# Performance work log

Measured on AMD Instinct MI355X. Metric: run time of the kernel, lower is better.

## Reference

```python
import jax, jax.numpy as jnp
import numpy as np

B, N, IN_DIM, OUT_DIM, H = 4, 2048, 1024, 1024, 16
HEAD_DIM = OUT_DIM // H  # 64


def setup_inputs() -> dict:
    key = jax.random.key(0)
    k_x, k_q, k_k, k_v, k_o = jax.random.split(key, 5)
    s = 1.0 / np.sqrt(IN_DIM)
    return {
        "x": jax.random.normal(k_x, (B, N, IN_DIM), dtype=jnp.float32),
        "w_q": jax.random.normal(k_q, (IN_DIM, OUT_DIM), dtype=jnp.float32) * s,
        "w_k": jax.random.normal(k_k, (IN_DIM, OUT_DIM), dtype=jnp.float32) * s,
        "w_v": jax.random.normal(k_v, (IN_DIM, OUT_DIM), dtype=jnp.float32) * s,
        "w_out": jax.random.normal(k_o, (OUT_DIM, OUT_DIM), dtype=jnp.float32) * s,
    }


def reference(x, w_q, w_k, w_v, w_out):
    b, n, _ = x.shape
    scale = 1.0 / jnp.sqrt(jnp.float32(HEAD_DIM))
    # QKV projections, split into heads: [b, h, n, d]
    q = (x @ w_q).reshape(b, n, H, HEAD_DIM).transpose(0, 2, 1, 3)
    k = (x @ w_k).reshape(b, n, H, HEAD_DIM).transpose(0, 2, 1, 3)
    v = (x @ w_v).reshape(b, n, H, HEAD_DIM).transpose(0, 2, 1, 3)
    # full score matrix [b, h, q, k]
    scores = jnp.einsum("bhqd,bhkd->bhqk", q, k) * scale
    # NOTE: source applies softmax over dim=1 (the HEAD axis) — reproduce exactly
    attn = jax.nn.softmax(scores, axis=1)
    # dropout p=0.0 -> identity
    ctx = jnp.einsum("bhqk,bhkd->bqhd", attn, v).reshape(b, n, OUT_DIM)
    return ctx @ w_out
```

## Files before the change

kernel.cpp:

```cpp
#include <hip/hip_runtime.h>
#include <hip/hip_bf16.h>

typedef unsigned short u16;
typedef unsigned int u32;
typedef __attribute__((ext_vector_type(8))) short short8;
typedef __attribute__((ext_vector_type(4))) float float4v;
typedef __attribute__((ext_vector_type(4))) unsigned int uint4v;

__device__ __forceinline__ u16 f2bf(float f) {
    union { float f; unsigned int u; } v; v.f = f;
    unsigned int r = v.u + 0x7fffu + ((v.u >> 16) & 1u);
    return (u16)(r >> 16);
}
__device__ __forceinline__ float bf2f(u16 h) {
    union { unsigned int u; float f; } v; v.u = ((unsigned int)h) << 16;
    return v.f;
}

__device__ __forceinline__ void gld_lds16(const u16* g, u16* l) {
    __builtin_amdgcn_global_load_lds(
        (const __attribute__((address_space(1))) u32*)g,
        (__attribute__((address_space(3))) u32*)l, 16, 0, 0);
}

__global__ __launch_bounds__(256) void convert_x(
    const float* __restrict__ x, u16* __restrict__ xb) {
    int i = (blockIdx.x * 256 + threadIdx.x) * 8;
    float4v a = *(const float4v*)&x[i];
    float4v b = *(const float4v*)&x[i + 4];
    u16 tmp[8] __attribute__((aligned(16)));
#pragma unroll
    for (int j = 0; j < 4; ++j) { tmp[j] = f2bf(a[j]); tmp[4 + j] = f2bf(b[j]); }
    *(uint4v*)&xb[i] = *(uint4v*)tmp;
}

__global__ __launch_bounds__(256) void transpose_w(
    const float* __restrict__ w0, const float* __restrict__ w1,
    const float* __restrict__ w2, const float* __restrict__ w3,
    u16* __restrict__ o0, u16* __restrict__ o1,
    u16* __restrict__ o2, u16* __restrict__ o3) {
    __shared__ u16 t[32][33];
    int z = blockIdx.z;
    const float* w = (z == 0) ? w0 : (z == 1) ? w1 : (z == 2) ? w2 : w3;
    u16* o         = (z == 0) ? o0 : (z == 1) ? o1 : (z == 2) ? o2 : o3;
    int bx = blockIdx.x * 32;
    int by = blockIdx.y * 32;
    int x = threadIdx.x, y = threadIdx.y;
#pragma unroll
    for (int i = 0; i < 4; ++i)
        t[y + i * 8][x] = f2bf(w[(size_t)(by + y + i * 8) * 1024 + bx + x]);
    __syncthreads();
#pragma unroll
    for (int i = 0; i < 4; ++i)
        o[(size_t)(bx + y + i * 8) * 1024 + by + x] = t[x][y + i * 8];
}

__global__ __launch_bounds__(256) void gemm_bt(
    const u16* __restrict__ A, const u16* __restrict__ Bt,
    void* __restrict__ Cout, int M, int N, int K, int mode) {
    __shared__ __attribute__((aligned(16))) u16 As[128 * 32];
    __shared__ __attribute__((aligned(16))) u16 Bs[128 * 32];
    const int tid = threadIdx.x;
    const int m0 = blockIdx.y * 128;
    const int n0 = blockIdx.x * 128;
    const int wid = tid >> 6;
    const int lane = tid & 63;
    const int ln = lane & 15, kq = lane >> 4;
    const int wm = (wid >> 1) * 64, wn = (wid & 1) * 64;

    float4v acc[4][4] = {};
    for (int k0 = 0; k0 < K; k0 += 32) {
#pragma unroll
        for (int i = 0; i < 2; ++i) {
            int chunk = tid + i * 256;
            int row = chunk >> 2, cg = chunk & 3;
            u16* lA = &As[(size_t)(i * 256 + wid * 64) * 8];
            u16* lB = &Bs[(size_t)(i * 256 + wid * 64) * 8];
            gld_lds16(&A[(size_t)(m0 + row) * K + k0 + cg * 8], lA);
            gld_lds16(&Bt[(size_t)(n0 + row) * K + k0 + cg * 8], lB);
        }
        __syncthreads();
        short8 af[4], bfr[4];
#pragma unroll
        for (int mt = 0; mt < 4; ++mt)
            af[mt] = *(const short8*)&As[(wm + mt * 16 + ln) * 32 + kq * 8];
#pragma unroll
        for (int nt = 0; nt < 4; ++nt)
            bfr[nt] = *(const short8*)&Bs[(wn + nt * 16 + ln) * 32 + kq * 8];
#pragma unroll
        for (int mt = 0; mt < 4; ++mt)
#pragma unroll
            for (int nt = 0; nt < 4; ++nt)
                acc[mt][nt] = __builtin_amdgcn_mfma_f32_16x16x32_bf16(
                    af[mt], bfr[nt], acc[mt][nt], 0, 0, 0);
        __syncthreads();
    }
    if (mode == 0) {
        u16* C = (u16*)Cout;
#pragma unroll
        for (int mt = 0; mt < 4; ++mt)
#pragma unroll
            for (int nt = 0; nt < 4; ++nt)
#pragma unroll
                for (int r = 0; r < 4; ++r) {
                    int row = m0 + wm + mt * 16 + kq * 4 + r;
                    int col = n0 + wn + nt * 16 + ln;
                    C[(size_t)row * N + col] = f2bf(acc[mt][nt][r]);
                }
    } else if (mode == 1) {
        u16* C = (u16*)Cout;
#pragma unroll
        for (int mt = 0; mt < 4; ++mt)
#pragma unroll
            for (int nt = 0; nt < 4; ++nt)
#pragma unroll
                for (int r = 0; r < 4; ++r) {
                    int t = m0 + wm + mt * 16 + kq * 4 + r;
                    int col = n0 + wn + nt * 16 + ln;
                    int b = t >> 11, n = t & 2047;
                    C[((size_t)(b * 1024 + col)) * 2048 + n] = f2bf(acc[mt][nt][r]);
                }
    } else {
        float* C = (float*)Cout;
#pragma unroll
        for (int mt = 0; mt < 4; ++mt)
#pragma unroll
            for (int nt = 0; nt < 4; ++nt)
#pragma unroll
                for (int r = 0; r < 4; ++r) {
                    int row = m0 + wm + mt * 16 + kq * 4 + r;
                    int col = n0 + wn + nt * 16 + ln;
                    C[(size_t)row * N + col] = acc[mt][nt][r];
                }
    }
}

__global__ __launch_bounds__(1024) void attn_kernel(
    const u16* qb, const u16* __restrict__ kb,
    const u16* __restrict__ vt, u16* cb) {
    __shared__ __attribute__((aligned(16))) u16 E[2][16 * 32 * 40];
    __shared__ float Di[32 * 36];

    const int b = blockIdx.y;
    const int q0 = blockIdx.x * 32;
    const int tid = threadIdx.x;
    const int wid = tid >> 6, lane = tid & 63;
    const int ln = lane & 15, kq = lane >> 4;
    const int h = wid;

    short8 aq[2][2];
#pragma unroll
    for (int mt = 0; mt < 2; ++mt)
#pragma unroll
        for (int kc = 0; kc < 2; ++kc)
            aq[mt][kc] = *(const short8*)&qb[
                (size_t)(b * 2048 + q0 + mt * 16 + ln) * 1024 +
                h * 64 + kc * 32 + kq * 8];

    float4v cacc[2][4] = {};

#pragma unroll 1
    for (int kt = 0; kt < 2048; kt += 32) {
        const int cur = (kt >> 5) & 1;
        short8 bk[2][2];
        short8 bv[4];
#pragma unroll
        for (int kc = 0; kc < 2; ++kc)
#pragma unroll
            for (int nt = 0; nt < 2; ++nt)
                bk[kc][nt] = *(const short8*)&kb[
                    (size_t)(b * 2048 + kt + nt * 16 + ln) * 1024 +
                    h * 64 + kc * 32 + kq * 8];
#pragma unroll
        for (int nt = 0; nt < 4; ++nt)
            bv[nt] = *(const short8*)&vt[
                (size_t)(b * 1024 + h * 64 + nt * 16 + ln) * 2048 + kt + kq * 8];

        float4v sacc[2][2] = {};
#pragma unroll
        for (int kc = 0; kc < 2; ++kc)
#pragma unroll
            for (int mt = 0; mt < 2; ++mt)
#pragma unroll
                for (int nt = 0; nt < 2; ++nt)
                    sacc[mt][nt] = __builtin_amdgcn_mfma_f32_16x16x32_bf16(
                        aq[mt][kc], bk[kc][nt], sacc[mt][nt], 0, 0, 0);

#pragma unroll
        for (int mt = 0; mt < 2; ++mt)
#pragma unroll
            for (int nt = 0; nt < 2; ++nt)
#pragma unroll
                for (int r = 0; r < 4; ++r) {
                    float s = sacc[mt][nt][r] * 0.18033688f;
                    E[cur][(h * 32 + mt * 16 + kq * 4 + r) * 40 + nt * 16 + ln] =
                        f2bf(exp2f(fminf(s, 115.0f)));
                }
        __syncthreads();

        {
            int q = tid >> 5, kk = tid & 31;
            float d = 0.f;
#pragma unroll
            for (int hh = 0; hh < 16; ++hh)
                d += bf2f(E[cur][(hh * 32 + q) * 40 + kk]);
            Di[q * 36 + kk] = __builtin_amdgcn_rcpf(d);
        }
        __syncthreads();

        short8 ap[2];
#pragma unroll
        for (int mt = 0; mt < 2; ++mt) {
            const u16* ep = &E[cur][(h * 32 + mt * 16 + ln) * 40 + kq * 8];
            const float* dp = &Di[(mt * 16 + ln) * 36 + kq * 8];
            u16 tmp[8] __attribute__((aligned(16)));
#pragma unroll
            for (int j = 0; j < 8; ++j)
                tmp[j] = f2bf(bf2f(ep[j]) * dp[j]);
            ap[mt] = *(short8*)tmp;
        }
#pragma unroll
        for (int nt = 0; nt < 4; ++nt)
#pragma unroll
            for (int mt = 0; mt < 2; ++mt)
                cacc[mt][nt] = __builtin_amdgcn_mfma_f32_16x16x32_bf16(
                    ap[mt], bv[nt], cacc[mt][nt], 0, 0, 0);
    }

#pragma unroll
    for (int mt = 0; mt < 2; ++mt)
#pragma unroll
        for (int nt = 0; nt < 4; ++nt)
#pragma unroll
            for (int r = 0; r < 4; ++r) {
                int row = b * 2048 + q0 + mt * 16 + kq * 4 + r;
                int col = h * 64 + nt * 16 + ln;
                cb[(size_t)row * 1024 + col] = f2bf(cacc[mt][nt][r]);
            }
}

extern "C" void kernel_launch(void* const* d_in, const int* in_sizes, int n_in,
                              void* d_out, int out_size, void* d_ws, size_t ws_size,
                              hipStream_t stream) {
    const float* x   = (const float*)d_in[0];
    const float* w_q = (const float*)d_in[1];
    const float* w_k = (const float*)d_in[2];
    const float* w_v = (const float*)d_in[3];
    const float* w_o = (const float*)d_in[4];

    char* ws = (char*)d_ws;
    const size_t SZ_W   = (size_t)1024 * 1024 * 2;
    const size_t SZ_TOK = (size_t)8192 * 1024 * 2;
    u16* x_bf  = (u16*)(ws);
    u16* wtq   = (u16*)(ws + SZ_TOK);
    u16* wtk   = (u16*)(ws + SZ_TOK + SZ_W);
    u16* wtv   = (u16*)(ws + SZ_TOK + 2 * SZ_W);
    u16* wto   = (u16*)(ws + SZ_TOK + 3 * SZ_W);
    u16* q_buf = (u16*)(ws + SZ_TOK + 4 * SZ_W);
    u16* k_buf  = (u16*)d_out;
    u16* vt_buf = (u16*)d_out + (size_t)8192 * 1024;

    convert_x<<<4096, 256, 0, stream>>>(x, x_bf);

    transpose_w<<<dim3(32, 32, 4), dim3(32, 8), 0, stream>>>(
        w_q, w_k, w_v, w_o, wtq, wtk, wtv, wto);

    gemm_bt<<<dim3(8, 64), 256, 0, stream>>>(x_bf, wtq, q_buf, 8192, 1024, 1024, 0);
    gemm_bt<<<dim3(8, 64), 256, 0, stream>>>(x_bf, wtk, k_buf, 8192, 1024, 1024, 0);
    gemm_bt<<<dim3(8, 64), 256, 0, stream>>>(x_bf, wtv, vt_buf, 8192, 1024, 1024, 1);

    attn_kernel<<<dim3(64, 4), 1024, 0, stream>>>(q_buf, k_buf, vt_buf, q_buf);

    gemm_bt<<<dim3(8, 64), 256, 0, stream>>>(q_buf, wto, d_out, 8192, 1024, 1024, 2);
}
```

Baseline: 511.0 us.

## Halve attention query tile, keep exp scores in fp32 LDS, fold scale into Q GEMM

The attention kernel now handles 16 queries per block instead of 32, doubling the grid to 512 blocks, and adds an occupancy hint to launch_bounds. Exponentiated scores are stored to LDS as fp32 with vectorized writes, via a transposed MFMA (K as the A operand), rather than as scalar bf16 stores. The head-sum reduction uses half the threads with four partial accumulators. Normalized probabilities are packed with v_cvt_pk_bf16_f32, and the softmax scale is folded into the Q projection epilogue. The aim is better parallelism and less LDS and conversion overhead, at the cost of reloading each K/V tile twice as often across blocks.

```diff
diff --git a/kernel.cpp b/kernel.cpp
--- a/kernel.cpp
+++ b/kernel.cpp
@@ -12,9 +12,11 @@
     unsigned int r = v.u + 0x7fffu + ((v.u >> 16) & 1u);
     return (u16)(r >> 16);
 }
-__device__ __forceinline__ float bf2f(u16 h) {
-    union { unsigned int u; float f; } v; v.u = ((unsigned int)h) << 16;
-    return v.f;
+
+__device__ __forceinline__ u32 cvtpk(float lo, float hi) {
+    u32 r;
+    asm("v_cvt_pk_bf16_f32 %0, %1, %2" : "=v"(r) : "v"(lo), "v"(hi));
+    return r;
 }
 
 __device__ __forceinline__ void gld_lds16(const u16* g, u16* l) {
@@ -57,7 +59,7 @@
 
 __global__ __launch_bounds__(256) void gemm_bt(
     const u16* __restrict__ A, const u16* __restrict__ Bt,
-    void* __restrict__ Cout, int M, int N, int K, int mode) {
+    void* __restrict__ Cout, int M, int N, int K, int mode, float oscale) {
     __shared__ __attribute__((aligned(16))) u16 As[128 * 32];
     __shared__ __attribute__((aligned(16))) u16 Bs[128 * 32];
     const int tid = threadIdx.x;
@@ -105,7 +107,7 @@
                 for (int r = 0; r < 4; ++r) {
                     int row = m0 + wm + mt * 16 + kq * 4 + r;
                     int col = n0 + wn + nt * 16 + ln;
-                    C[(size_t)row * N + col] = f2bf(acc[mt][nt][r]);
+                    C[(size_t)row * N + col] = f2bf(acc[mt][nt][r] * oscale);
                 }
     } else if (mode == 1) {
         u16* C = (u16*)Cout;
@@ -135,35 +137,33 @@
     }
 }
 
-__global__ __launch_bounds__(1024) void attn_kernel(
+__global__ __launch_bounds__(1024, 8) void attn_kernel(
     const u16* qb, const u16* __restrict__ kb,
     const u16* __restrict__ vt, u16* cb) {
-    __shared__ __attribute__((aligned(16))) u16 E[2][16 * 32 * 40];
-    __shared__ float Di[32 * 36];
+    __shared__ __attribute__((aligned(16))) float Ef[2][256 * 36];
+    __shared__ __attribute__((aligned(16))) float Di[16 * 36];
 
     const int b = blockIdx.y;
-    const int q0 = blockIdx.x * 32;
+    const int q0 = blockIdx.x * 16;
     const int tid = threadIdx.x;
     const int wid = tid >> 6, lane = tid & 63;
     const int ln = lane & 15, kq = lane >> 4;
     const int h = wid;
 
-    short8 aq[2][2];
-#pragma unroll
-    for (int mt = 0; mt < 2; ++mt)
-#pragma unroll
-        for (int kc = 0; kc < 2; ++kc)
-            aq[mt][kc] = *(const short8*)&qb[
-                (size_t)(b * 2048 + q0 + mt * 16 + ln) * 1024 +
-                h * 64 + kc * 32 + kq * 8];
-
-    float4v cacc[2][4] = {};
+    short8 aq[2];
+#pragma unroll
+    for (int kc = 0; kc < 2; ++kc)
+        aq[kc] = *(const short8*)&qb[
+            (size_t)(b * 2048 + q0 + ln) * 1024 + h * 64 + kc * 32 + kq * 8];
+
+    float4v cacc[4] = {};
 
 #pragma unroll 1
     for (int kt = 0; kt < 2048; kt += 32) {
         const int cur = (kt >> 5) & 1;
+        float* E = Ef[cur];
+
         short8 bk[2][2];
-        short8 bv[4];
 #pragma unroll
         for (int kc = 0; kc < 2; ++kc)
 #pragma unroll
@@ -171,72 +171,73 @@
                 bk[kc][nt] = *(const short8*)&kb[
                     (size_t)(b * 2048 + kt + nt * 16 + ln) * 1024 +
                     h * 64 + kc * 32 + kq * 8];
+
+        float4v sacc[2] = {};
+#pragma unroll
+        for (int kc = 0; kc < 2; ++kc)
+#pragma unroll
+            for (int nt = 0; nt < 2; ++nt)
+                sacc[nt] = __builtin_amdgcn_mfma_f32_16x16x32_bf16(
+                    bk[kc][nt], aq[kc], sacc[nt], 0, 0, 0);
+
+#pragma unroll
+        for (int nt = 0; nt < 2; ++nt) {
+            float4v e;
+#pragma unroll
+            for (int r = 0; r < 4; ++r)
+                e[r] = exp2f(fminf(sacc[nt][r], 115.0f));
+            *(float4v*)&E[(h * 16 + ln) * 36 + nt * 16 + kq * 4] = e;
+        }
+
+        short8 bv[4];
 #pragma unroll
         for (int nt = 0; nt < 4; ++nt)
             bv[nt] = *(const short8*)&vt[
                 (size_t)(b * 1024 + h * 64 + nt * 16 + ln) * 2048 + kt + kq * 8];
 
-        float4v sacc[2][2] = {};
-#pragma unroll
-        for (int kc = 0; kc < 2; ++kc)
-#pragma unroll
-            for (int mt = 0; mt < 2; ++mt)
-#pragma unroll
-                for (int nt = 0; nt < 2; ++nt)
-                    sacc[mt][nt] = __builtin_amdgcn_mfma_f32_16x16x32_bf16(
-                        aq[mt][kc], bk[kc][nt], sacc[mt][nt], 0, 0, 0);
-
-#pragma unroll
-        for (int mt = 0; mt < 2; ++mt)
-#pragma unroll
-            for (int nt = 0; nt < 2; ++nt)
-#pragma unroll
-                for (int r = 0; r < 4; ++r) {
-                    float s = sacc[mt][nt][r] * 0.18033688f;
-                    E[cur][(h * 32 + mt * 16 + kq * 4 + r) * 40 + nt * 16 + ln] =
-                        f2bf(exp2f(fminf(s, 115.0f)));
-                }
-        __syncthreads();
-
-        {
-            int q = tid >> 5, kk = tid & 31;
-            float d = 0.f;
-#pragma unroll
-            for (int hh = 0; hh < 16; ++hh)
-                d += bf2f(E[cur][(hh * 32 + q) * 40 + kk]);
-            Di[q * 36 + kk] = __builtin_amdgcn_rcpf(d);
-        }
-        __syncthreads();
-
-        short8 ap[2];
-#pragma unroll
-        for (int mt = 0; mt < 2; ++mt) {
-            const u16* ep = &E[cur][(h * 32 + mt * 16 + ln) * 40 + kq * 8];
-            const float* dp = &Di[(mt * 16 + ln) * 36 + kq * 8];
-            u16 tmp[8] __attribute__((aligned(16)));
-#pragma unroll
-            for (int j = 0; j < 8; ++j)
-                tmp[j] = f2bf(bf2f(ep[j]) * dp[j]);
-            ap[mt] = *(short8*)tmp;
-        }
+        __syncthreads();
+
+        if (tid < 512) {
+            const int q = tid >> 5, kk = tid & 31;
+            const float* ec = &E[q * 36 + kk];
+            float d0 = 0.f, d1 = 0.f, d2 = 0.f, d3 = 0.f;
+#pragma unroll
+            for (int hh = 0; hh < 4; ++hh) {
+                d0 += ec[(hh * 4 + 0) * (16 * 36)];
+                d1 += ec[(hh * 4 + 1) * (16 * 36)];
+                d2 += ec[(hh * 4 + 2) * (16 * 36)];
+                d3 += ec[(hh * 4 + 3) * (16 * 36)];
+            }
+            Di[q * 36 + kk] = __builtin_amdgcn_rcpf((d0 + d1) + (d2 + d3));
+        }
+        __syncthreads();
+
+        const float* ep = &E[(h * 16 + ln) * 36 + kq * 8];
+        const float* dp = &Di[ln * 36 + kq * 8];
+        float4v e0 = *(const float4v*)&ep[0];
+        float4v e1 = *(const float4v*)&ep[4];
+        float4v g0 = *(const float4v*)&dp[0];
+        float4v g1 = *(const float4v*)&dp[4];
+        u32 pk[4] __attribute__((aligned(16)));
+        pk[0] = cvtpk(e0[0] * g0[0], e0[1] * g0[1]);
+        pk[1] = cvtpk(e0[2] * g0[2], e0[3] * g0[3]);
+        pk[2] = cvtpk(e1[0] * g1[0], e1[1] * g1[1]);
+        pk[3] = cvtpk(e1[2] * g1[2], e1[3] * g1[3]);
+        short8 ap = *(short8*)pk;
 #pragma unroll
         for (int nt = 0; nt < 4; ++nt)
-#pragma unroll
-            for (int mt = 0; mt < 2; ++mt)
-                cacc[mt][nt] = __builtin_amdgcn_mfma_f32_16x16x32_bf16(
-                    ap[mt], bv[nt], cacc[mt][nt], 0, 0, 0);
+            cacc[nt] = __builtin_amdgcn_mfma_f32_16x16x32_bf16(
+                ap, bv[nt], cacc[nt], 0, 0, 0);
     }
 
 #pragma unroll
-    for (int mt = 0; mt < 2; ++mt)
-#pragma unroll
-        for (int nt = 0; nt < 4; ++nt)
-#pragma unroll
-            for (int r = 0; r < 4; ++r) {
-                int row = b * 2048 + q0 + mt * 16 + kq * 4 + r;
-                int col = h * 64 + nt * 16 + ln;
-                cb[(size_t)row * 1024 + col] = f2bf(cacc[mt][nt][r]);
-            }
+    for (int nt = 0; nt < 4; ++nt)
+#pragma unroll
+        for (int r = 0; r < 4; ++r) {
+            int row = b * 2048 + q0 + kq * 4 + r;
+            int col = h * 64 + nt * 16 + ln;
+            cb[(size_t)row * 1024 + col] = f2bf(cacc[nt][r]);
+        }
 }
 
 extern "C" void kernel_launch(void* const* d_in, const int* in_sizes, int n_in,
@@ -265,11 +266,11 @@
     transpose_w<<<dim3(32, 32, 4), dim3(32, 8), 0, stream>>>(
         w_q, w_k, w_v, w_o, wtq, wtk, wtv, wto);
 
-    gemm_bt<<<dim3(8, 64), 256, 0, stream>>>(x_bf, wtq, q_buf, 8192, 1024, 1024, 0);
-    gemm_bt<<<dim3(8, 64), 256, 0, stream>>>(x_bf, wtk, k_buf, 8192, 1024, 1024, 0);
-    gemm_bt<<<dim3(8, 64), 256, 0, stream>>>(x_bf, wtv, vt_buf, 8192, 1024, 1024, 1);
-
-    attn_kernel<<<dim3(64, 4), 1024, 0, stream>>>(q_buf, k_buf, vt_buf, q_buf);
-
-    gemm_bt<<<dim3(8, 64), 256, 0, stream>>>(q_buf, wto, d_out, 8192, 1024, 1024, 2);
-}
+    gemm_bt<<<dim3(8, 64), 256, 0, stream>>>(x_bf, wtq, q_buf, 8192, 1024, 1024, 0, 0.18033688f);
+    gemm_bt<<<dim3(8, 64), 256, 0, stream>>>(x_bf, wtk, k_buf, 8192, 1024, 1024, 0, 1.0f);
+    gemm_bt<<<dim3(8, 64), 256, 0, stream>>>(x_bf, wtv, vt_buf, 8192, 1024, 1024, 1, 1.0f);
+
+    attn_kernel<<<dim3(128, 4), 1024, 0, stream>>>(q_buf, k_buf, vt_buf, q_buf);
+
+    gemm_bt<<<dim3(8, 64), 256, 0, stream>>>(q_buf, wto, d_out, 8192, 1024, 1024, 2, 1.0f);
+}
```

After: 864.1 us. 69.1% more time.
